# Kernel optimization log

Hardware: AMD Instinct MI355X
Metric: run time of the kernel (lower is better)

Reference implementation:

```python
import jax, jax.numpy as jnp
import numpy as np

D_MODEL = 1024
H = 16
D_K = D_MODEL // H
B = 2
S = 2048


def setup_inputs() -> dict:
    key = jax.random.key(0)
    ks = jax.random.split(key, 11)
    scale = 1.0 / np.sqrt(D_MODEL)
    inp = {
        "query": jax.random.normal(ks[0], (B, S, D_MODEL), jnp.float32),
        "key_in": jax.random.normal(ks[1], (B, S, D_MODEL), jnp.float32),
        "value": jax.random.normal(ks[2], (B, S, D_MODEL), jnp.float32),
        # causal mask, broadcast over heads: 1 = keep, 0 = masked
        "mask": jnp.tril(jnp.ones((S, S), jnp.int32))[None, None, :, :].repeat(B, axis=0),
        "w_q": jax.random.normal(ks[3], (D_MODEL, D_MODEL), jnp.float32) * scale,
        "b_q": jax.random.normal(ks[4], (D_MODEL,), jnp.float32) * 0.01,
        "w_k": jax.random.normal(ks[5], (D_MODEL, D_MODEL), jnp.float32) * scale,
        "b_k": jax.random.normal(ks[6], (D_MODEL,), jnp.float32) * 0.01,
        "w_v": jax.random.normal(ks[7], (D_MODEL, D_MODEL), jnp.float32) * scale,
        "b_v": jax.random.normal(ks[8], (D_MODEL,), jnp.float32) * 0.01,
        "w_out": jax.random.normal(ks[9], (D_MODEL, D_MODEL), jnp.float32) * scale,
        "b_out": jax.random.normal(ks[10], (D_MODEL,), jnp.float32) * 0.01,
    }
    return inp


def _split_heads(x):
    # [B,S,D] -> [B,H,S,d_k]
    b, s, _ = x.shape
    return x.reshape(b, s, H, D_K).transpose(0, 2, 1, 3)


def reference(query, key_in, value, mask, w_q, b_q, w_k, b_k, w_v, b_v, w_out, b_out):
    q = _split_heads(query @ w_q.T + b_q)
    k = _split_heads(key_in @ w_k.T + b_k)
    v = _split_heads(value @ w_v.T + b_v)
    scores = jnp.einsum("bhqd,bhkd->bhqk", q, k) / jnp.sqrt(jnp.float32(D_K))
    scores = jnp.where(mask == 0, jnp.float32(-1e9), scores)
    attn = jax.nn.softmax(scores, axis=-1)  # dropout rate 0.0 -> identity
    out = jnp.einsum("bhqk,bhkd->bhqd", attn, v)
    out = out.transpose(0, 2, 1, 3).reshape(query.shape[0], -1, D_MODEL)
    return out @ w_out.T + b_out
```

## Files before the change

### kernel.cpp

```cpp
#include <hip/hip_runtime.h>
#include <hip/hip_bf16.h>
#include <type_traits>

#define D_MODEL 1024
#define NH 16
#define DKH 64
#define BB 2
#define SS 2048
#define MTOT (BB * SS)

typedef __hip_bfloat16 bf16;
typedef __attribute__((ext_vector_type(8))) short short8;
typedef __attribute__((ext_vector_type(4))) short short4v;
typedef __attribute__((ext_vector_type(4))) float floatx4;

__device__ __forceinline__ bf16 f2bf(float x) { return __float2bfloat16(x); }

__device__ __forceinline__ void async_cp16(const void* g, void* l) {
  __builtin_amdgcn_global_load_lds(
      (const __attribute__((address_space(1))) unsigned int*)g,
      (__attribute__((address_space(3))) unsigned int*)l, 16, 0, 0);
}

__global__ __launch_bounds__(256) void convert_w_kernel(
    const float* __restrict__ wq, const float* __restrict__ wk,
    const float* __restrict__ wv, const float* __restrict__ wo,
    bf16* __restrict__ out) {
  const int id = blockIdx.x * 256 + threadIdx.x;
  const int m = id >> 18;
  const int loc = id & 262143;
  const float* src = (m == 0) ? wq : (m == 1) ? wk : (m == 2) ? wv : wo;
  const float4 v = *(const float4*)(src + (size_t)loc * 4);
  short4v s;
  bf16* pb = (bf16*)&s;
  pb[0] = f2bf(v.x); pb[1] = f2bf(v.y); pb[2] = f2bf(v.z); pb[3] = f2bf(v.w);
  *(short4v*)(out + ((size_t)m << 20) + (size_t)loc * 4) = s;
}

template <typename TIN>
__device__ __forceinline__ void gemm_body(const TIN* __restrict__ A,
                                          const bf16* __restrict__ W,
                                          const float* __restrict__ Bi,
                                          void* __restrict__ Cv, int mode) {
  constexpr int N = 1024, K = 1024;
  __shared__ TIN As[2][128 * 32];
  __shared__ bf16 Ws[2][128 * 32];

  const int tid = threadIdx.x;
  const int w = tid >> 6, lane = tid & 63, quad = lane >> 4, n16 = lane & 15;
  const int bx = blockIdx.x;
  const int bm = bx & 31, bn = bx >> 5;
  const int wm = (w & 1) * 64, wn = (w >> 1) * 64;

  const int rf = lane >> 3, cf = lane & 7;
  const int rb = lane >> 2, cb = lane & 3;

  const bf16* Wg0 = W + (size_t)(bn * 128) * K;

  auto issue = [&](int buf, int k0) {
    if constexpr (std::is_same<TIN, float>::value) {
      const float* Ag = (const float*)A + (size_t)(bm * 128) * K + k0;
#pragma unroll
      for (int ii = 0; ii < 4; ii++) {
        const int R = w * 32 + ii * 8 + rf;
        async_cp16(Ag + (size_t)R * K + ((cf ^ (R & 7)) * 4),
                   (void*)&As[buf][(w * 32 + ii * 8) * 32]);
      }
    } else {
      const bf16* Ag = (const bf16*)A + (size_t)(bm * 128) * K + k0;
#pragma unroll
      for (int ii = 0; ii < 2; ii++) {
        const int R = w * 32 + ii * 16 + rb;
        async_cp16(Ag + (size_t)R * K + cb * 8,
                   (void*)&As[buf][(w * 32 + ii * 16) * 32]);
      }
    }
    const bf16* Wg = Wg0 + k0;
#pragma unroll
    for (int ii = 0; ii < 2; ii++) {
      const int R = w * 32 + ii * 16 + rb;
      async_cp16(Wg + (size_t)R * K + cb * 8,
                 (void*)&Ws[buf][(w * 32 + ii * 16) * 32]);
    }
  };

  floatx4 acc[4][4] = {};
  issue(0, 0);
  int buf = 0;
  for (int k0 = 0; k0 < K; k0 += 32) {
    __syncthreads();
    if (k0 + 32 < K) issue(buf ^ 1, k0 + 32);

    short8 af[4], bfr[4];
#pragma unroll
    for (int i = 0; i < 4; i++) {
      const int Rr = wm + i * 16 + n16;
      if constexpr (std::is_same<TIN, float>::value) {
        const float* ap = (const float*)&As[buf][Rr * 32];
        const float4 f0 = *(const float4*)(ap + (((quad * 2 + 0) ^ (Rr & 7)) * 4));
        const float4 f1 = *(const float4*)(ap + (((quad * 2 + 1) ^ (Rr & 7)) * 4));
        bf16* pb = (bf16*)&af[i];
        pb[0] = f2bf(f0.x); pb[1] = f2bf(f0.y); pb[2] = f2bf(f0.z); pb[3] = f2bf(f0.w);
        pb[4] = f2bf(f1.x); pb[5] = f2bf(f1.y); pb[6] = f2bf(f1.z); pb[7] = f2bf(f1.w);
      } else {
        af[i] = *(const short8*)((const bf16*)&As[buf][Rr * 32] + quad * 8);
      }
    }
#pragma unroll
    for (int j = 0; j < 4; j++)
      bfr[j] = *(const short8*)(&Ws[buf][(wn + j * 16 + n16) * 32 + quad * 8]);
#pragma unroll
    for (int i = 0; i < 4; i++)
#pragma unroll
      for (int j = 0; j < 4; j++)
        acc[i][j] = __builtin_amdgcn_mfma_f32_16x16x32_bf16(af[i], bfr[j], acc[i][j], 0, 0, 0);
    buf ^= 1;
  }

  float bv[4];
#pragma unroll
  for (int j = 0; j < 4; j++) bv[j] = Bi[bn * 128 + wn + j * 16 + n16];

#pragma unroll
  for (int i = 0; i < 4; i++) {
    const int rowb = bm * 128 + wm + i * 16 + quad * 4;
#pragma unroll
    for (int j = 0; j < 4; j++) {
      const int col = bn * 128 + wn + j * 16 + n16;
      if (mode == 1) {
        short4v s;
        bf16* pb = (bf16*)&s;
#pragma unroll
        for (int r = 0; r < 4; r++) pb[r] = f2bf(acc[i][j][r] + bv[j]);
        *(short4v*)((bf16*)Cv + (size_t)col * MTOT + rowb) = s;
      } else if (mode == 0) {
        bf16* C = (bf16*)Cv;
#pragma unroll
        for (int r = 0; r < 4; r++)
          C[(size_t)(rowb + r) * N + col] = f2bf(acc[i][j][r] + bv[j]);
      } else {
        float* C = (float*)Cv;
#pragma unroll
        for (int r = 0; r < 4; r++)
          C[(size_t)(rowb + r) * N + col] = acc[i][j][r] + bv[j];
      }
    }
  }
}

__global__ __launch_bounds__(256) void gemm_qkv_kernel(
    const float* __restrict__ q_in, const float* __restrict__ k_in,
    const float* __restrict__ v_in, const bf16* __restrict__ Wb,
    const float* __restrict__ bq, const float* __restrict__ bk,
    const float* __restrict__ bv, bf16* __restrict__ Qw,
    bf16* __restrict__ Kw, bf16* __restrict__ VTw) {
  const int z = blockIdx.z;
  const float* A = (z == 0) ? q_in : (z == 1) ? k_in : v_in;
  const bf16* W = Wb + ((size_t)z << 20);
  const float* Bi = (z == 0) ? bq : (z == 1) ? bk : bv;
  void* C = (z == 0) ? (void*)Qw : (z == 1) ? (void*)Kw : (void*)VTw;
  gemm_body<float>(A, W, Bi, C, (z == 2) ? 1 : 0);
}

__global__ __launch_bounds__(256) void gemm_out_kernel(
    const bf16* __restrict__ A, const bf16* __restrict__ W,
    const float* __restrict__ Bi, float* __restrict__ C) {
  gemm_body<bf16>(A, W, Bi, (void*)C, 2);
}

__global__ __launch_bounds__(256) void attn_kernel(const bf16* __restrict__ Q,
                                                   const bf16* __restrict__ Kg,
                                                   const bf16* __restrict__ VT,
                                                   bf16* __restrict__ O) {
  constexpr int BN = 128, LDK = 72, LDV = 136, LDP = 136;
  __shared__ bf16 Ks[128 * LDK];
  __shared__ bf16 Vs[64 * LDV];
  __shared__ bf16 Pw[4 * 16 * LDP];

  const int tid = threadIdx.x;
  const int w = tid >> 6, lane = tid & 63, quad = lane >> 4, n16 = lane & 15;
  const int hb = blockIdx.x;
  const int h = hb & 15, b = hb >> 4, p = blockIdx.y;
  const size_t qoff = (size_t)b * SS * D_MODEL + h * DKH;
  const bf16* VTh = VT + (size_t)(h * DKH) * MTOT + (size_t)b * SS;

  const int kvr = tid >> 3, ck = tid & 7;
  const int dd = tid >> 4, cv = tid & 15;

  short8 kreg[4], vreg[4];
  auto loadKV = [&](int kv0) {
#pragma unroll
    for (int ii = 0; ii < 4; ii++) {
      kreg[ii] = *(const short8*)(Kg + qoff + (size_t)(kv0 + ii * 32 + kvr) * D_MODEL + ck * 8);
      vreg[ii] = *(const short8*)(VTh + (size_t)(ii * 16 + dd) * MTOT + kv0 + cv * 8);
    }
  };

  for (int hf = 0; hf < 2; hf++) {
    const int q0 = (hf == 0) ? p * 64 : (31 - p) * 64;
    const int q0w = q0 + w * 16;
    const int nt = (q0 + 191) >> 7;

    short8 aQ0, aQ1;
    {
      const bf16* qp = Q + qoff + (size_t)(q0w + n16) * D_MODEL + quad * 8;
      aQ0 = *(const short8*)(qp);
      aQ1 = *(const short8*)(qp + 32);
    }

    floatx4 facc[4] = {};
    float m_i[4], l_i[4];
#pragma unroll
    for (int r = 0; r < 4; r++) { m_i[r] = -1e30f; l_i[r] = 0.f; }

    loadKV(0);
    for (int t = 0; t < nt; t++) {
#pragma unroll
      for (int ii = 0; ii < 4; ii++) {
        *(short8*)(&Ks[(ii * 32 + kvr) * LDK + ck * 8]) = kreg[ii];
        *(short8*)(&Vs[(ii * 16 + dd) * LDV + cv * 8]) = vreg[ii];
      }
      __syncthreads();
      if (t + 1 < nt) loadKV((t + 1) * BN);

      const int kv0 = t * BN;
      float pv[8][4];
      float mt[4] = {-1e30f, -1e30f, -1e30f, -1e30f};
      const int qrow_base = q0w + quad * 4;
#pragma unroll
      for (int blk = 0; blk < 8; blk++) {
        floatx4 z = {};
        short8 bk0 = *(const short8*)(&Ks[(blk * 16 + n16) * LDK + quad * 8]);
        short8 bk1 = *(const short8*)(&Ks[(blk * 16 + n16) * LDK + 32 + quad * 8]);
        z = __builtin_amdgcn_mfma_f32_16x16x32_bf16(aQ0, bk0, z, 0, 0, 0);
        z = __builtin_amdgcn_mfma_f32_16x16x32_bf16(aQ1, bk1, z, 0, 0, 0);
        const int kvg = kv0 + blk * 16 + n16;
#pragma unroll
        for (int r = 0; r < 4; r++) {
          float s = z[r] * 0.125f;
          if (kvg > qrow_base + r) s = -1e30f;
          pv[blk][r] = s;
          mt[r] = fmaxf(mt[r], s);
        }
      }
#pragma unroll
      for (int off = 1; off < 16; off <<= 1)
#pragma unroll
        for (int r = 0; r < 4; r++) mt[r] = fmaxf(mt[r], __shfl_xor(mt[r], off, 64));

      float alpha[4];
#pragma unroll
      for (int r = 0; r < 4; r++) {
        const float mn = fmaxf(m_i[r], mt[r]);
        alpha[r] = __expf(m_i[r] - mn);
        m_i[r] = mn;
      }
      float rs[4] = {0.f, 0.f, 0.f, 0.f};
#pragma unroll
      for (int blk = 0; blk < 8; blk++)
#pragma unroll
        for (int r = 0; r < 4; r++) {
          const float pe = __expf(pv[blk][r] - m_i[r]);
          pv[blk][r] = pe;
          rs[r] += pe;
        }
#pragma unroll
      for (int off = 1; off < 16; off <<= 1)
#pragma unroll
        for (int r = 0; r < 4; r++) rs[r] += __shfl_xor(rs[r], off, 64);
#pragma unroll
      for (int r = 0; r < 4; r++) l_i[r] = l_i[r] * alpha[r] + rs[r];
#pragma unroll
      for (int d = 0; d < 4; d++)
#pragma unroll
        for (int r = 0; r < 4; r++) facc[d][r] *= alpha[r];

      bf16* pw = &Pw[w * 16 * LDP];
#pragma unroll
      for (int blk = 0; blk < 8; blk++)
#pragma unroll
        for (int r = 0; r < 4; r++)
          pw[(quad * 4 + r) * LDP + blk * 16 + n16] = f2bf(pv[blk][r]);

      short8 aP[4];
#pragma unroll
      for (int c = 0; c < 4; c++)
        aP[c] = *(const short8*)(&pw[n16 * LDP + c * 32 + quad * 8]);

#pragma unroll
      for (int d = 0; d < 4; d++)
#pragma unroll
        for (int c = 0; c < 4; c++) {
          short8 bvf = *(const short8*)(&Vs[(d * 16 + n16) * LDV + c * 32 + quad * 8]);
          facc[d] = __builtin_amdgcn_mfma_f32_16x16x32_bf16(aP[c], bvf, facc[d], 0, 0, 0);
        }
      __syncthreads();
    }

#pragma unroll
    for (int r = 0; r < 4; r++) {
      const float inv = 1.f / l_i[r];
      const int qrow = q0w + quad * 4 + r;
      bf16* op = O + qoff + (size_t)qrow * D_MODEL;
#pragma unroll
      for (int d = 0; d < 4; d++) op[d * 16 + n16] = f2bf(facc[d][r] * inv);
    }
  }
}

extern "C" void kernel_launch(void* const* d_in, const int* in_sizes, int n_in,
                              void* d_out, int out_size, void* d_ws, size_t ws_size,
                              hipStream_t stream) {
  (void)in_sizes; (void)n_in; (void)out_size; (void)ws_size;
  const float* query  = (const float*)d_in[0];
  const float* key_in = (const float*)d_in[1];
  const float* value  = (const float*)d_in[2];
  const float* w_q = (const float*)d_in[4];
  const float* b_q = (const float*)d_in[5];
  const float* w_k = (const float*)d_in[6];
  const float* b_k = (const float*)d_in[7];
  const float* w_v = (const float*)d_in[8];
  const float* b_v = (const float*)d_in[9];
  const float* w_o = (const float*)d_in[10];
  const float* b_o = (const float*)d_in[11];
  float* outp = (float*)d_out;

  const size_t mat = (size_t)MTOT * D_MODEL;
  bf16* Qws  = (bf16*)d_ws;
  bf16* Kws  = Qws + mat;
  bf16* VTws = Kws + mat;
  bf16* Wb   = VTws + mat;

  convert_w_kernel<<<4096, 256, 0, stream>>>(w_q, w_k, w_v, w_o, Wb);

  dim3 gq(256, 1, 3);
  gemm_qkv_kernel<<<gq, 256, 0, stream>>>(query, key_in, value, Wb, b_q, b_k,
                                          b_v, Qws, Kws, VTws);
  dim3 ga(NH * BB, 16);
  attn_kernel<<<ga, 256, 0, stream>>>(Qws, Kws, VTws, Qws);
  dim3 go(256, 1, 1);
  gemm_out_kernel<<<go, 256, 0, stream>>>(Qws, Wb + ((size_t)3 << 20), b_o, outp);
}
```

Baseline: 264.8 us.

## Stage fp32 A as bf16 via registers in QKV GEMM; shrink out-proj M tile

The QKV projection GEMM now loads fp32 activations into registers, converts them to bf16 and writes them to LDS, replacing async fp32 global-to-LDS copies with per-fragment conversion. This halves LDS footprint and read traffic for A, at the cost of register-staged (non-async) global loads. The output-projection GEMM becomes a dedicated kernel with 64x128 tiles and 512 blocks instead of 256, to fill more CUs on the machine. Each out-proj block now re-reads more of W relative to its output.

```diff
diff --git a/kernel.cpp b/kernel.cpp
--- a/kernel.cpp
+++ b/kernel.cpp
@@ -1,6 +1,5 @@
 #include <hip/hip_runtime.h>
 #include <hip/hip_bf16.h>
-#include <type_traits>
 
 #define D_MODEL 1024
 #define NH 16
@@ -37,13 +36,12 @@
   *(short4v*)(out + ((size_t)m << 20) + (size_t)loc * 4) = s;
 }
 
-template <typename TIN>
-__device__ __forceinline__ void gemm_body(const TIN* __restrict__ A,
-                                          const bf16* __restrict__ W,
-                                          const float* __restrict__ Bi,
-                                          void* __restrict__ Cv, int mode) {
+__device__ __forceinline__ void gemm_qkv_body(const float* __restrict__ A,
+                                              const bf16* __restrict__ W,
+                                              const float* __restrict__ Bi,
+                                              bf16* __restrict__ C, int mode) {
   constexpr int N = 1024, K = 1024;
-  __shared__ TIN As[2][128 * 32];
+  __shared__ bf16 As[2][128 * 32];
   __shared__ bf16 Ws[2][128 * 32];
 
   const int tid = threadIdx.x;
@@ -52,30 +50,30 @@
   const int bm = bx & 31, bn = bx >> 5;
   const int wm = (w & 1) * 64, wn = (w >> 1) * 64;
 
-  const int rf = lane >> 3, cf = lane & 7;
+  const int ra = tid >> 3, ca = tid & 7;
   const int rb = lane >> 2, cb = lane & 3;
 
+  const float* Af = A + (size_t)(bm * 128) * K;
   const bf16* Wg0 = W + (size_t)(bn * 128) * K;
 
-  auto issue = [&](int buf, int k0) {
-    if constexpr (std::is_same<TIN, float>::value) {
-      const float* Ag = (const float*)A + (size_t)(bm * 128) * K + k0;
-#pragma unroll
-      for (int ii = 0; ii < 4; ii++) {
-        const int R = w * 32 + ii * 8 + rf;
-        async_cp16(Ag + (size_t)R * K + ((cf ^ (R & 7)) * 4),
-                   (void*)&As[buf][(w * 32 + ii * 8) * 32]);
-      }
-    } else {
-      const bf16* Ag = (const bf16*)A + (size_t)(bm * 128) * K + k0;
-#pragma unroll
-      for (int ii = 0; ii < 2; ii++) {
-        const int R = w * 32 + ii * 16 + rb;
-        async_cp16(Ag + (size_t)R * K + cb * 8,
-                   (void*)&As[buf][(w * 32 + ii * 16) * 32]);
-      }
-    }
-    const bf16* Wg = Wg0 + k0;
+  float4 pa4[4];
+  auto loadA = [&](int kk) {
+#pragma unroll
+    for (int ii = 0; ii < 4; ii++)
+      pa4[ii] = *(const float4*)(Af + (size_t)(ii * 32 + ra) * K + kk + ca * 4);
+  };
+  auto stageA = [&](int buf) {
+#pragma unroll
+    for (int ii = 0; ii < 4; ii++) {
+      short4v s;
+      bf16* pb = (bf16*)&s;
+      pb[0] = f2bf(pa4[ii].x); pb[1] = f2bf(pa4[ii].y);
+      pb[2] = f2bf(pa4[ii].z); pb[3] = f2bf(pa4[ii].w);
+      *(short4v*)(&As[buf][(ii * 32 + ra) * 32 + ca * 4]) = s;
+    }
+  };
+  auto issueW = [&](int buf, int kk) {
+    const bf16* Wg = Wg0 + kk;
 #pragma unroll
     for (int ii = 0; ii < 2; ii++) {
       const int R = w * 32 + ii * 16 + rb;
@@ -85,27 +83,18 @@
   };
 
   floatx4 acc[4][4] = {};
-  issue(0, 0);
+  loadA(0);
+  issueW(0, 0);
   int buf = 0;
   for (int k0 = 0; k0 < K; k0 += 32) {
+    stageA(buf);
     __syncthreads();
-    if (k0 + 32 < K) issue(buf ^ 1, k0 + 32);
+    if (k0 + 32 < K) { loadA(k0 + 32); issueW(buf ^ 1, k0 + 32); }
 
     short8 af[4], bfr[4];
 #pragma unroll
-    for (int i = 0; i < 4; i++) {
-      const int Rr = wm + i * 16 + n16;
-      if constexpr (std::is_same<TIN, float>::value) {
-        const float* ap = (const float*)&As[buf][Rr * 32];
-        const float4 f0 = *(const float4*)(ap + (((quad * 2 + 0) ^ (Rr & 7)) * 4));
-        const float4 f1 = *(const float4*)(ap + (((quad * 2 + 1) ^ (Rr & 7)) * 4));
-        bf16* pb = (bf16*)&af[i];
-        pb[0] = f2bf(f0.x); pb[1] = f2bf(f0.y); pb[2] = f2bf(f0.z); pb[3] = f2bf(f0.w);
-        pb[4] = f2bf(f1.x); pb[5] = f2bf(f1.y); pb[6] = f2bf(f1.z); pb[7] = f2bf(f1.w);
-      } else {
-        af[i] = *(const short8*)((const bf16*)&As[buf][Rr * 32] + quad * 8);
-      }
-    }
+    for (int i = 0; i < 4; i++)
+      af[i] = *(const short8*)(&As[buf][(wm + i * 16 + n16) * 32 + quad * 8]);
 #pragma unroll
     for (int j = 0; j < 4; j++)
       bfr[j] = *(const short8*)(&Ws[buf][(wn + j * 16 + n16) * 32 + quad * 8]);
@@ -132,17 +121,11 @@
         bf16* pb = (bf16*)&s;
 #pragma unroll
         for (int r = 0; r < 4; r++) pb[r] = f2bf(acc[i][j][r] + bv[j]);
-        *(short4v*)((bf16*)Cv + (size_t)col * MTOT + rowb) = s;
-      } else if (mode == 0) {
-        bf16* C = (bf16*)Cv;
+        *(short4v*)(C + (size_t)col * MTOT + rowb) = s;
+      } else {
 #pragma unroll
         for (int r = 0; r < 4; r++)
           C[(size_t)(rowb + r) * N + col] = f2bf(acc[i][j][r] + bv[j]);
-      } else {
-        float* C = (float*)Cv;
-#pragma unroll
-        for (int r = 0; r < 4; r++)
-          C[(size_t)(rowb + r) * N + col] = acc[i][j][r] + bv[j];
       }
     }
   }
@@ -158,14 +141,77 @@
   const float* A = (z == 0) ? q_in : (z == 1) ? k_in : v_in;
   const bf16* W = Wb + ((size_t)z << 20);
   const float* Bi = (z == 0) ? bq : (z == 1) ? bk : bv;
-  void* C = (z == 0) ? (void*)Qw : (z == 1) ? (void*)Kw : (void*)VTw;
-  gemm_body<float>(A, W, Bi, C, (z == 2) ? 1 : 0);
+  bf16* C = (z == 0) ? Qw : (z == 1) ? Kw : VTw;
+  gemm_qkv_body(A, W, Bi, C, (z == 2) ? 1 : 0);
 }
 
 __global__ __launch_bounds__(256) void gemm_out_kernel(
     const bf16* __restrict__ A, const bf16* __restrict__ W,
     const float* __restrict__ Bi, float* __restrict__ C) {
-  gemm_body<bf16>(A, W, Bi, (void*)C, 2);
+  constexpr int N = 1024, K = 1024;
+  __shared__ bf16 As[2][64 * 32];
+  __shared__ bf16 Ws[2][128 * 32];
+
+  const int tid = threadIdx.x;
+  const int w = tid >> 6, lane = tid & 63, quad = lane >> 4, n16 = lane & 15;
+  const int bx = blockIdx.x;
+  const int bm = bx & 63, bn = bx >> 6;
+  const int wm = (w & 1) * 32, wn = (w >> 1) * 64;
+
+  const int rl = lane >> 2, cl = lane & 3;
+
+  const bf16* Ag0 = A + (size_t)(bm * 64) * K;
+  const bf16* Wg0 = W + (size_t)(bn * 128) * K;
+
+  auto issue = [&](int buf, int kk) {
+    async_cp16(Ag0 + (size_t)(w * 16 + rl) * K + kk + cl * 8,
+               (void*)&As[buf][(w * 16) * 32]);
+    const bf16* Wg = Wg0 + kk;
+#pragma unroll
+    for (int ii = 0; ii < 2; ii++) {
+      const int R = w * 32 + ii * 16 + rl;
+      async_cp16(Wg + (size_t)R * K + cl * 8,
+                 (void*)&Ws[buf][(w * 32 + ii * 16) * 32]);
+    }
+  };
+
+  floatx4 acc[2][4] = {};
+  issue(0, 0);
+  int buf = 0;
+  for (int k0 = 0; k0 < K; k0 += 32) {
+    __syncthreads();
+    if (k0 + 32 < K) issue(buf ^ 1, k0 + 32);
+
+    short8 af[2], bfr[4];
+#pragma unroll
+    for (int i = 0; i < 2; i++)
+      af[i] = *(const short8*)(&As[buf][(wm + i * 16 + n16) * 32 + quad * 8]);
+#pragma unroll
+    for (int j = 0; j < 4; j++)
+      bfr[j] = *(const short8*)(&Ws[buf][(wn + j * 16 + n16) * 32 + quad * 8]);
+#pragma unroll
+    for (int i = 0; i < 2; i++)
+#pragma unroll
+      for (int j = 0; j < 4; j++)
+        acc[i][j] = __builtin_amdgcn_mfma_f32_16x16x32_bf16(af[i], bfr[j], acc[i][j], 0, 0, 0);
+    buf ^= 1;
+  }
+
+  float bv[4];
+#pragma unroll
+  for (int j = 0; j < 4; j++) bv[j] = Bi[bn * 128 + wn + j * 16 + n16];
+
+#pragma unroll
+  for (int i = 0; i < 2; i++) {
+    const int rowb = bm * 64 + wm + i * 16 + quad * 4;
+#pragma unroll
+    for (int j = 0; j < 4; j++) {
+      const int col = bn * 128 + wn + j * 16 + n16;
+#pragma unroll
+      for (int r = 0; r < 4; r++)
+        C[(size_t)(rowb + r) * N + col] = acc[i][j][r] + bv[j];
+    }
+  }
 }
 
 __global__ __launch_bounds__(256) void attn_kernel(const bf16* __restrict__ Q,
@@ -338,6 +384,5 @@
                                           b_v, Qws, Kws, VTws);
   dim3 ga(NH * BB, 16);
   attn_kernel<<<ga, 256, 0, stream>>>(Qws, Kws, VTws, Qws);
-  dim3 go(256, 1, 1);
-  gemm_out_kernel<<<go, 256, 0, stream>>>(Qws, Wb + ((size_t)3 << 20), b_o, outp);
-}
+  gemm_out_kernel<<<512, 256, 0, stream>>>(Qws, Wb + ((size_t)3 << 20), b_o, outp);
+}
```

Result: slower. 275.7 us (+4.1%).
